# Optimization experiments

Measured on AMD Instinct MI355X. Metric: run time of the kernel, lower is better.

## Reference

```python
import jax, jax.numpy as jnp
import numpy as np

HEADS = 16
DIM_HEAD = 64


def rotate_half(t):
    x1, x2 = jnp.split(t, 2, axis=-1)
    return jnp.concatenate((-x2, x1), axis=-1)


def apply_rotary_pos_emb(t, freqs):
    # t: [b, h, n, l], freqs: [n, l]
    seq_len = t.shape[-2]
    freqs = freqs[-seq_len:, :]
    return t * jnp.cos(freqs) + rotate_half(t) * jnp.sin(freqs)


def setup_inputs() -> dict:
    key = jax.random.key(0)
    ks = jax.random.split(key, 6)
    b, n, dim, l = 2, 2048, 1024, 32
    x = jax.random.normal(ks[0], (b, n, dim), dtype=jnp.float32)
    rotary_pos_emb = jax.random.normal(ks[1], (n, l), dtype=jnp.float32)
    s = 0.02
    Wq = jax.random.normal(ks[2], (dim, dim), dtype=jnp.float32) * s
    Wk = jax.random.normal(ks[3], (dim, dim), dtype=jnp.float32) * s
    Wv = jax.random.normal(ks[4], (dim, dim), dtype=jnp.float32) * s
    Wout = jax.random.normal(ks[5], (dim, dim), dtype=jnp.float32) * s
    return {"x": x, "rotary_pos_emb": rotary_pos_emb, "Wq": Wq, "Wk": Wk, "Wv": Wv, "Wout": Wout}


def reference(x, rotary_pos_emb, Wq, Wk, Wv, Wout):
    b, n, _ = x.shape
    h, d = HEADS, DIM_HEAD
    scale = d ** -0.5

    def to_heads(t):
        return t.reshape(b, n, h, d).transpose(0, 2, 1, 3)  # b h n d

    q = to_heads(x @ Wq)
    k = to_heads(x @ Wk)
    v = to_heads(x @ Wv)

    # partial rotary on first l dims of q, k, v (module applies rope to v too)
    l = rotary_pos_emb.shape[-1]

    def rope(t):
        tl, tr = t[..., :l], t[..., l:]
        return jnp.concatenate((apply_rotary_pos_emb(tl, rotary_pos_emb), tr), axis=-1)

    q, k, v = rope(q), rope(k), rope(v)

    dots = jnp.einsum('bhid,bhjd->bhij', q, k) * scale  # [b, h, n, n]
    mask_value = jnp.finfo(dots.dtype).min
    causal = jnp.triu(jnp.ones((n, n), dtype=bool), k=1)  # i < j
    dots = jnp.where(causal[None, None, :, :], mask_value, dots)

    attn = jax.nn.softmax(dots, axis=-1)
    out = jnp.einsum('bhij,bhjd->bhid', attn, v)
    out = out.transpose(0, 2, 1, 3).reshape(b, n, h * d)  # b n (h d)
    return out @ Wout
```

## Files before the change

### kernel.cpp

```cpp
#include <hip/hip_runtime.h>
#include <hip/hip_bf16.h>
#include <stdint.h>

#define BATCH 2
#define SEQ 2048
#define NHEADS 16
#define DIM 1024
#define MTOT 4096
#define LOG2E 1.4426950408889634f
#define QSCALE (0.125f * LOG2E)
#define DEFER_THR 11.54f

typedef __attribute__((ext_vector_type(8))) short s16x8;
typedef __attribute__((ext_vector_type(4))) float f32x4;
typedef unsigned short u16;

__device__ __forceinline__ u16 f2b(float f) {
  union { float f; uint32_t u; } v; v.f = f;
  uint32_t r = v.u + 0x7FFFu + ((v.u >> 16) & 1u);
  return (u16)(r >> 16);
}
__device__ __forceinline__ u16 f2b_fast(float f) {
  union { float f; uint32_t u; } v; v.f = f;
  return (u16)((v.u + 0x8000u) >> 16);
}
__device__ __forceinline__ float b2f(u16 h) {
  union { uint32_t u; float f; } v; v.u = ((uint32_t)h) << 16;
  return v.f;
}

__device__ __forceinline__ void gload_lds16(void* lds, const void* g) {
  __builtin_amdgcn_global_load_lds(
      (const __attribute__((address_space(1))) unsigned int*)g,
      (__attribute__((address_space(3))) unsigned int*)lds, 16, 0, 0);
}

__global__ __launch_bounds__(256) void prep_kernel(
    const float* __restrict__ x, const float* __restrict__ Wq,
    const float* __restrict__ Wk, const float* __restrict__ Wv,
    const float* __restrict__ Wo, const float* __restrict__ rot,
    u16* __restrict__ xb, u16* __restrict__ WtAll, float2* __restrict__ cs) {
  __shared__ float tile[32][33];
  int bid = blockIdx.x, t = threadIdx.x;
  if (bid < 4096) {
    int i = (bid * 256 + t) * 4;
    float4 v = *(const float4*)(x + i);
    ushort4 o;
    o.x = f2b(v.x); o.y = f2b(v.y); o.z = f2b(v.z); o.w = f2b(v.w);
    *(ushort4*)(xb + i) = o;
  } else if (bid < 8192) {
    int bb = bid - 4096;
    int z = bb >> 10, xB = bb & 31, yB = (bb >> 5) & 31;
    const float* W = (z == 0) ? Wq : (z == 1) ? Wk : (z == 2) ? Wv : Wo;
    u16* Wt = WtAll + (size_t)z * DIM * DIM;
    int k0 = xB * 32, n0 = yB * 32;
    int tx = t & 31, ty = t >> 5;
#pragma unroll
    for (int i = 0; i < 4; i++) {
      int r = ty + i * 8;
      tile[r][tx] = W[(size_t)(k0 + r) * DIM + n0 + tx];
    }
    __syncthreads();
#pragma unroll
    for (int i = 0; i < 4; i++) {
      int r = ty + i * 8;
      Wt[(size_t)(n0 + r) * DIM + k0 + tx] = f2b(tile[tx][r]);
    }
  } else {
    int i = (bid - 8192) * 256 + t;
    float f = rot[i];
    float s, c;
    __sincosf(f, &s, &c);
    cs[i] = make_float2(c, s);
  }
}

template <int MODE>
__global__ __launch_bounds__(256) void gemm128(
    const u16* __restrict__ A, const u16* __restrict__ BtBase,
    void* __restrict__ Cbase, const float2* __restrict__ cs,
    u16* __restrict__ Qh, u16* __restrict__ Kh, u16* __restrict__ Vt) {
  __shared__ u16 Asm[2][128 * 32];
  __shared__ u16 Bsm[2][128 * 32];
  const u16* Bt = BtBase + (size_t)blockIdx.z * DIM * DIM;

  int t = threadIdx.x;
  int w = t >> 6, l = t & 63;
  int wr = w >> 1, wc = w & 1;
  int lr = l & 15, lg = l >> 4;
  int rowBase = blockIdx.x * 128;
  int colBase = blockIdx.y * 128;

  const char* Ab = (const char*)(A + (size_t)rowBase * DIM);
  const char* Bb = (const char*)(Bt + (size_t)colBase * DIM);

  f32x4 acc[4][4];
#pragma unroll
  for (int m = 0; m < 4; m++)
#pragma unroll
    for (int n = 0; n < 4; n++) acc[m][n] = (f32x4){0.f, 0.f, 0.f, 0.f};

  auto stage = [&](int buf, int kt) {
#pragma unroll
    for (int i = 0; i < 2; i++) {
      int ob = t * 16 + i * 4096;
      int row = ob >> 6, cb = ob & 63;
      int src = row * (DIM * 2) + kt * 64 + (cb ^ (((row >> 1) & 3) << 4));
      gload_lds16((char*)&Asm[buf][0] + ob, Ab + src);
      gload_lds16((char*)&Bsm[buf][0] + ob, Bb + src);
    }
  };

  stage(0, 0);
  for (int kt = 0; kt < DIM / 32; ++kt) {
    int cur = kt & 1;
    __syncthreads();
    if (kt + 1 < DIM / 32) stage(cur ^ 1, kt + 1);
    const char* ab = (const char*)&Asm[cur][0];
    const char* bb = (const char*)&Bsm[cur][0];
    s16x8 af[4], bf[4];
#pragma unroll
    for (int m = 0; m < 4; m++) {
      int R = wr * 64 + m * 16 + lr;
      af[m] = *(const s16x8*)(ab + R * 64 + ((lg * 16) ^ (((R >> 1) & 3) << 4)));
    }
#pragma unroll
    for (int n = 0; n < 4; n++) {
      int R = wc * 64 + n * 16 + lr;
      bf[n] = *(const s16x8*)(bb + R * 64 + ((lg * 16) ^ (((R >> 1) & 3) << 4)));
    }
    __builtin_amdgcn_s_setprio(1);
#pragma unroll
    for (int m = 0; m < 4; m++)
#pragma unroll
      for (int n = 0; n < 4; n++)
        acc[m][n] = __builtin_amdgcn_mfma_f32_16x16x32_bf16(af[m], bf[n], acc[m][n], 0, 0, 0);
    __builtin_amdgcn_s_setprio(0);
  }

  if constexpr (MODE == 1) {
    float* C = (float*)Cbase;
#pragma unroll
    for (int m = 0; m < 4; m++)
#pragma unroll
      for (int n = 0; n < 4; n++) {
        int row = rowBase + wr * 64 + m * 16 + lg * 4;
        int col = colBase + wc * 64 + n * 16 + lr;
#pragma unroll
        for (int r = 0; r < 4; r++)
          C[(size_t)(row + r) * DIM + col] = acc[m][n][r];
      }
  } else {
    int z = blockIdx.z;
    int h = (colBase + wc * 64) >> 6;
    if (z == 2) {
#pragma unroll
      for (int m = 0; m < 4; m++) {
#pragma unroll
        for (int r = 0; r < 4; r++) {
          int row = rowBase + wr * 64 + m * 16 + lg * 4 + r;
          int nrow = row & (SEQ - 1);
          int b2 = row >> 11;
          const float2* csr = cs + (size_t)nrow * 32;
          float a0 = acc[m][0][r], a1 = acc[m][1][r];
          float2 f0 = csr[lr];
          float2 f1 = csr[16 + lr];
          float o0 = a0 * f0.x - a1 * f0.y;
          float o1 = a1 * f1.x + a0 * f1.y;
          size_t vbase = ((size_t)(b2 * NHEADS + h) * 64) * SEQ + nrow;
          Vt[vbase + (size_t)lr * SEQ]        = f2b(o0);
          Vt[vbase + (size_t)(16 + lr) * SEQ] = f2b(o1);
          Vt[vbase + (size_t)(32 + lr) * SEQ] = f2b(acc[m][2][r]);
          Vt[vbase + (size_t)(48 + lr) * SEQ] = f2b(acc[m][3][r]);
        }
      }
    } else {
      u16* C = (z == 0) ? Qh : Kh;
      float sc = (z == 0) ? QSCALE : 1.0f;
#pragma unroll
      for (int m = 0; m < 4; m++) {
#pragma unroll
        for (int r = 0; r < 4; r++) {
          int row = rowBase + wr * 64 + m * 16 + lg * 4 + r;
          int nrow = row & (SEQ - 1);
          int b2 = row >> 11;
          const float2* csr = cs + (size_t)nrow * 32;
          float a0 = acc[m][0][r], a1 = acc[m][1][r];
          float2 f0 = csr[lr];
          float2 f1 = csr[16 + lr];
          float o0 = (a0 * f0.x - a1 * f0.y) * sc;
          float o1 = (a1 * f1.x + a0 * f1.y) * sc;
          size_t base = ((size_t)(b2 * NHEADS + h) * SEQ + nrow) * 64;
          C[base + lr]      = f2b(o0);
          C[base + 16 + lr] = f2b(o1);
          C[base + 32 + lr] = f2b(acc[m][2][r] * sc);
          C[base + 48 + lr] = f2b(acc[m][3][r] * sc);
        }
      }
    }
  }
}

__global__ __launch_bounds__(256) void attn_kernel(
    const u16* __restrict__ Qh, const u16* __restrict__ Kh,
    const u16* __restrict__ Vtg, u16* __restrict__ Ob) {
  int id = blockIdx.x;
  int xcd = id & 7, within = id >> 3;
  int bh = xcd * 4 + (within >> 4);
  int pi = within & 15;
  int b = bh >> 4, h = bh & 15;
  __shared__ u16 Ks[2][64 * 64];
  __shared__ u16 Vs[2][64 * 64];
  __shared__ u16 Ps[4][16 * 64];
  int t = threadIdx.x, w = t >> 6, l = t & 63;
  int lr = l & 15, lg = l >> 4;
  char* psb = (char*)&Ps[w][0];

  const char* Kbh = (const char*)(Kh + (size_t)bh * SEQ * 64);
  const char* Vbh = (const char*)Vtg + (size_t)bh * 64 * SEQ * 2;
  const u16* Qbh = Qh + (size_t)bh * SEQ * 64;

  auto stage = [&](int buf, int kt) {
    const char* kg = Kbh + (size_t)kt * 64 * 128;
    const char* vg = Vbh + kt * 128;
#pragma unroll
    for (int i = 0; i < 2; i++) {
      int ob = i * 4096 + t * 16;
      int row = ob >> 7, cb = ob & 127;
      int sw = cb ^ ((row & 7) << 4);
      gload_lds16((char*)&Ks[buf][0] + ob, kg + row * 128 + sw);
      gload_lds16((char*)&Vs[buf][0] + ob, vg + row * 4096 + sw);
    }
  };

#pragma unroll 1
  for (int ph = 0; ph < 2; ++ph) {
    int qt = ph ? (31 - pi) : pi;
    int nkt = qt + 1;
    int qrow0 = qt * 64 + w * 16;

    s16x8 qf[2];
#pragma unroll
    for (int kk = 0; kk < 2; kk++)
      qf[kk] = *(const s16x8*)(Qbh + (size_t)(qrow0 + lr) * 64 + kk * 32 + lg * 8);

    f32x4 o[4];
#pragma unroll
    for (int n = 0; n < 4; n++) o[n] = (f32x4){0.f, 0.f, 0.f, 0.f};
    float mrun[4], lsum[4];
#pragma unroll
    for (int r = 0; r < 4; r++) { mrun[r] = -3.0e38f; lsum[r] = 0.f; }

    __syncthreads();
    stage(0, 0);
    for (int kt = 0; kt < nkt; ++kt) {
      int cur = kt & 1;
      __syncthreads();
      if (kt + 1 < nkt) stage(cur ^ 1, kt + 1);
      const char* kb = (const char*)&Ks[cur][0];
      const char* vb = (const char*)&Vs[cur][0];

      f32x4 s[4];
#pragma unroll
      for (int n = 0; n < 4; n++) s[n] = (f32x4){0.f, 0.f, 0.f, 0.f};
      __builtin_amdgcn_s_setprio(1);
#pragma unroll
      for (int n = 0; n < 4; n++)
#pragma unroll
        for (int kk = 0; kk < 2; kk++) {
          int R = n * 16 + lr;
          s16x8 bk = *(const s16x8*)(kb + R * 128 + ((kk * 64 + lg * 16) ^ ((R & 7) << 4)));
          s[n] = __builtin_amdgcn_mfma_f32_16x16x32_bf16(qf[kk], bk, s[n], 0, 0, 0);
        }
      __builtin_amdgcn_s_setprio(0);

      if (kt == nkt - 1) {
#pragma unroll
        for (int n = 0; n < 4; n++) {
          int colg = kt * 64 + n * 16 + lr;
#pragma unroll
          for (int r = 0; r < 4; r++) {
            int rowg = qt * 64 + w * 16 + lg * 4 + r;
            if (colg > rowg) s[n][r] = -3.0e38f;
          }
        }
      }

      float tl[4];
#pragma unroll
      for (int r = 0; r < 4; r++)
        tl[r] = fmaxf(fmaxf(s[0][r], s[1][r]), fmaxf(s[2][r], s[3][r]));
      float need = fmaxf(fmaxf(tl[0] - mrun[0], tl[1] - mrun[1]),
                         fmaxf(tl[2] - mrun[2], tl[3] - mrun[3]));
      if (!__all(need <= DEFER_THR)) {
        float tm[4];
#pragma unroll
        for (int r = 0; r < 4; r++) tm[r] = tl[r];
#pragma unroll
        for (int off = 1; off < 16; off <<= 1)
#pragma unroll
          for (int r = 0; r < 4; r++) tm[r] = fmaxf(tm[r], __shfl_xor(tm[r], off, 64));
        float alpha[4];
#pragma unroll
        for (int r = 0; r < 4; r++) {
          float mn = fmaxf(mrun[r], tm[r]);
          alpha[r] = exp2f(mrun[r] - mn);
          mrun[r] = mn;
          lsum[r] *= alpha[r];
        }
#pragma unroll
        for (int n = 0; n < 4; n++)
#pragma unroll
          for (int r = 0; r < 4; r++) o[n][r] *= alpha[r];
      }
#pragma unroll
      for (int n = 0; n < 4; n++) {
#pragma unroll
        for (int r = 0; r < 4; r++) {
          float p = exp2f(s[n][r] - mrun[r]);
          lsum[r] += p;
          int prow = lg * 4 + r;
          *(u16*)(psb + prow * 128 + (((n * 16 + lr) * 2) ^ ((prow & 7) << 4))) = f2b_fast(p);
        }
      }

      s16x8 pa[2];
#pragma unroll
      for (int kk = 0; kk < 2; kk++)
        pa[kk] = *(const s16x8*)(psb + lr * 128 + ((kk * 64 + lg * 16) ^ ((lr & 7) << 4)));
      __builtin_amdgcn_s_setprio(1);
#pragma unroll
      for (int n = 0; n < 4; n++)
#pragma unroll
        for (int kk = 0; kk < 2; kk++) {
          int R = n * 16 + lr;
          s16x8 vv = *(const s16x8*)(vb + R * 128 + ((kk * 64 + lg * 16) ^ ((R & 7) << 4)));
          o[n] = __builtin_amdgcn_mfma_f32_16x16x32_bf16(pa[kk], vv, o[n], 0, 0, 0);
        }
      __builtin_amdgcn_s_setprio(0);
    }

#pragma unroll
    for (int off = 1; off < 16; off <<= 1)
#pragma unroll
      for (int r = 0; r < 4; r++) lsum[r] += __shfl_xor(lsum[r], off, 64);
    float inv[4];
#pragma unroll
    for (int r = 0; r < 4; r++) inv[r] = 1.0f / lsum[r];
#pragma unroll
    for (int n = 0; n < 4; n++)
#pragma unroll
      for (int r = 0; r < 4; r++) {
        int rowg = qt * 64 + w * 16 + lg * 4 + r;
        int col = h * 64 + n * 16 + lr;
        Ob[((size_t)b * SEQ + rowg) * DIM + col] = f2b(o[n][r] * inv[r]);
      }
  }
}

extern "C" void kernel_launch(void* const* d_in, const int* in_sizes, int n_in,
                              void* d_out, int out_size, void* d_ws, size_t ws_size,
                              hipStream_t stream) {
  (void)in_sizes; (void)n_in; (void)out_size; (void)ws_size;
  const float* x = (const float*)d_in[0];
  const float* rot = (const float*)d_in[1];
  const float* Wq = (const float*)d_in[2];
  const float* Wk = (const float*)d_in[3];
  const float* Wv = (const float*)d_in[4];
  const float* Wo = (const float*)d_in[5];

  char* ws = (char*)d_ws;
  u16* xb    = (u16*)(ws);
  u16* WtAll = (u16*)(ws + (8ll << 20));
  u16* Qh    = (u16*)(ws + (16ll << 20));
  u16* Kh    = (u16*)(ws + (24ll << 20));
  u16* Vt    = (u16*)(ws + (32ll << 20));
  u16* Ob    = (u16*)(ws + (40ll << 20));
  float2* cs = (float2*)(ws + (48ll << 20));

  prep_kernel<<<8448, 256, 0, stream>>>(x, Wq, Wk, Wv, Wo, rot, xb, WtAll, cs);
  gemm128<0><<<dim3(32, 8, 3), 256, 0, stream>>>(xb, WtAll, nullptr, cs, Qh, Kh, Vt);
  attn_kernel<<<512, 256, 0, stream>>>(Qh, Kh, Vt, Ob);
  gemm128<1><<<dim3(32, 8, 1), 256, 0, stream>>>(Ob, WtAll + 3ll * DIM * DIM, d_out,
                                                 nullptr, nullptr, nullptr, nullptr);
}
```

Measured before the change: 212.5 us.

## Replace QKV GEMM with 256x256-tile 8-wave pipelined kernel

The fused QKV projection now uses a dedicated kernel with 256x256 output tiles, 512 threads and a K-step of 64. Each K-step is split into half-tile stages that are issued interleaved with the MFMA phases under explicit barriers and vmcnt waits. The grid shrinks from 768 to 192 blocks, and each block treats the three weight matrices as one 3072-wide B operand. This is meant to raise data reuse per LDS load and overlap global loads with compute. The cost is fewer blocks than the 256 CUs on the device, so the single wave of work may leave CUs idle, along with higher register and LDS pressure.

After: 199.5 us. -6.1%, faster.

```diff
diff --git a/kernel.cpp b/kernel.cpp
--- a/kernel.cpp
+++ b/kernel.cpp
@@ -75,22 +75,181 @@
   }
 }
 
-template <int MODE>
-__global__ __launch_bounds__(256) void gemm128(
-    const u16* __restrict__ A, const u16* __restrict__ BtBase,
-    void* __restrict__ Cbase, const float2* __restrict__ cs,
-    u16* __restrict__ Qh, u16* __restrict__ Kh, u16* __restrict__ Vt) {
+#define NKT 16
+__global__ __launch_bounds__(512, 2) void qkv8_kernel(
+    const u16* __restrict__ A, const u16* __restrict__ Bt,
+    const float2* __restrict__ cs, u16* __restrict__ Qh,
+    u16* __restrict__ Kh, u16* __restrict__ Vt) {
+  __shared__ u16 lds[2][4][8192];
+  const int t = threadIdx.x;
+  const int w = t >> 6, l = t & 63;
+  const int wr = w >> 2, wc = w & 3;
+  const int lr = l & 15, lg = l >> 4;
+  const int rowBase = blockIdx.x * 256;
+  const int colBase = blockIdx.y * 256;
+  const char* Ab = (const char*)(A + (size_t)rowBase * DIM);
+  const char* Bb = (const char*)(Bt + (size_t)colBase * DIM);
+  const int t16 = t * 16;
+  const int swz = ((lr >> 1) & 3) << 4;
+
+  f32x4 acc[8][4];
+#pragma unroll
+  for (int m = 0; m < 8; m++)
+#pragma unroll
+    for (int n = 0; n < 4; n++) acc[m][n] = (f32x4){0.f, 0.f, 0.f, 0.f};
+
+  auto stageH = [&](int buf, int kind, int kt) {
+    const char* gb = (kind >= 2) ? Bb : Ab;
+    int khalf = kind & 1;
+    char* ldst = (char*)&lds[buf][kind][0];
+#pragma unroll
+    for (int i = 0; i < 2; i++) {
+      int ob = t16 + i * 8192;
+      int row = ob >> 6, cb = ob & 63;
+      gload_lds16(ldst + ob,
+                  gb + (size_t)row * (DIM * 2) + kt * 128 + khalf * 64 +
+                      (cb ^ (((row >> 1) & 3) << 4)));
+    }
+  };
+  auto rdA = [&](int cur, int m, int kk) -> s16x8 {
+    int R = wr * 128 + m * 16 + lr;
+    return *(const s16x8*)((const char*)&lds[cur][kk][0] + R * 64 + ((lg * 16) ^ swz));
+  };
+  auto rdB = [&](int cur, int n, int kk) -> s16x8 {
+    int R = wc * 64 + n * 16 + lr;
+    return *(const s16x8*)((const char*)&lds[cur][2 + kk][0] + R * 64 + ((lg * 16) ^ swz));
+  };
+
+  stageH(0, 0, 0); stageH(0, 2, 0); stageH(0, 1, 0); stageH(0, 3, 0);
+  stageH(1, 2, 1); stageH(1, 0, 1); stageH(1, 3, 1);
+
+  for (int kt = 0; kt < NKT; ++kt) {
+    const int cur = kt & 1, nxt = cur ^ 1;
+    if (kt >= NKT - 2) { asm volatile("s_waitcnt vmcnt(0)" ::: "memory"); }
+    else               { asm volatile("s_waitcnt vmcnt(6)" ::: "memory"); }
+    __builtin_amdgcn_s_barrier();
+    __builtin_amdgcn_sched_barrier(0);
+
+    s16x8 af[4], bf[4];
+#pragma unroll
+    for (int i = 0; i < 4; i++) { af[i] = rdA(cur, i, 0); bf[i] = rdB(cur, i, 0); }
+    if (kt + 1 < NKT) stageH(nxt, 1, kt + 1);
+    __builtin_amdgcn_s_barrier();
+    __builtin_amdgcn_sched_barrier(0);
+    __builtin_amdgcn_s_setprio(1);
+#pragma unroll
+    for (int m = 0; m < 4; m++)
+#pragma unroll
+      for (int n = 0; n < 4; n++)
+        acc[m][n] = __builtin_amdgcn_mfma_f32_16x16x32_bf16(af[m], bf[n], acc[m][n], 0, 0, 0);
+    __builtin_amdgcn_s_setprio(0);
+    __builtin_amdgcn_s_barrier();
+    __builtin_amdgcn_sched_barrier(0);
+#pragma unroll
+    for (int i = 0; i < 4; i++) af[i] = rdA(cur, 4 + i, 0);
+    if (kt + 2 < NKT) stageH(cur, 2, kt + 2);
+    __builtin_amdgcn_s_barrier();
+    __builtin_amdgcn_sched_barrier(0);
+    __builtin_amdgcn_s_setprio(1);
+#pragma unroll
+    for (int m = 0; m < 4; m++)
+#pragma unroll
+      for (int n = 0; n < 4; n++)
+        acc[4 + m][n] = __builtin_amdgcn_mfma_f32_16x16x32_bf16(af[m], bf[n], acc[4 + m][n], 0, 0, 0);
+    __builtin_amdgcn_s_setprio(0);
+    __builtin_amdgcn_s_barrier();
+    __builtin_amdgcn_sched_barrier(0);
+#pragma unroll
+    for (int i = 0; i < 4; i++) { af[i] = rdA(cur, i, 1); bf[i] = rdB(cur, i, 1); }
+    if (kt + 2 < NKT) stageH(cur, 0, kt + 2);
+    __builtin_amdgcn_s_barrier();
+    __builtin_amdgcn_sched_barrier(0);
+    __builtin_amdgcn_s_setprio(1);
+#pragma unroll
+    for (int m = 0; m < 4; m++)
+#pragma unroll
+      for (int n = 0; n < 4; n++)
+        acc[m][n] = __builtin_amdgcn_mfma_f32_16x16x32_bf16(af[m], bf[n], acc[m][n], 0, 0, 0);
+    __builtin_amdgcn_s_setprio(0);
+    __builtin_amdgcn_s_barrier();
+    __builtin_amdgcn_sched_barrier(0);
+#pragma unroll
+    for (int i = 0; i < 4; i++) af[i] = rdA(cur, 4 + i, 1);
+    if (kt + 2 < NKT) stageH(cur, 3, kt + 2);
+    __builtin_amdgcn_s_barrier();
+    __builtin_amdgcn_sched_barrier(0);
+    __builtin_amdgcn_s_setprio(1);
+#pragma unroll
+    for (int m = 0; m < 4; m++)
+#pragma unroll
+      for (int n = 0; n < 4; n++)
+        acc[4 + m][n] = __builtin_amdgcn_mfma_f32_16x16x32_bf16(af[m], bf[n], acc[4 + m][n], 0, 0, 0);
+    __builtin_amdgcn_s_setprio(0);
+    __builtin_amdgcn_s_barrier();
+    __builtin_amdgcn_sched_barrier(0);
+  }
+
+  int cg = colBase + wc * 64;
+  int z = cg >> 10;
+  int h = (cg >> 6) & (NHEADS - 1);
+  if (z == 2) {
+#pragma unroll
+    for (int m = 0; m < 8; m++) {
+#pragma unroll
+      for (int r = 0; r < 4; r++) {
+        int row = rowBase + wr * 128 + m * 16 + lg * 4 + r;
+        int nrow = row & (SEQ - 1);
+        int b2 = row >> 11;
+        const float2* csr = cs + (size_t)nrow * 32;
+        float a0 = acc[m][0][r], a1 = acc[m][1][r];
+        float2 f0 = csr[lr];
+        float2 f1 = csr[16 + lr];
+        float o0 = a0 * f0.x - a1 * f0.y;
+        float o1 = a1 * f1.x + a0 * f1.y;
+        size_t vbase = ((size_t)(b2 * NHEADS + h) * 64) * SEQ + nrow;
+        Vt[vbase + (size_t)lr * SEQ]        = f2b(o0);
+        Vt[vbase + (size_t)(16 + lr) * SEQ] = f2b(o1);
+        Vt[vbase + (size_t)(32 + lr) * SEQ] = f2b(acc[m][2][r]);
+        Vt[vbase + (size_t)(48 + lr) * SEQ] = f2b(acc[m][3][r]);
+      }
+    }
+  } else {
+    u16* C = (z == 0) ? Qh : Kh;
+    float sc = (z == 0) ? QSCALE : 1.0f;
+#pragma unroll
+    for (int m = 0; m < 8; m++) {
+#pragma unroll
+      for (int r = 0; r < 4; r++) {
+        int row = rowBase + wr * 128 + m * 16 + lg * 4 + r;
+        int nrow = row & (SEQ - 1);
+        int b2 = row >> 11;
+        const float2* csr = cs + (size_t)nrow * 32;
+        float a0 = acc[m][0][r], a1 = acc[m][1][r];
+        float2 f0 = csr[lr];
+        float2 f1 = csr[16 + lr];
+        float o0 = (a0 * f0.x - a1 * f0.y) * sc;
+        float o1 = (a1 * f1.x + a0 * f1.y) * sc;
+        size_t base = ((size_t)(b2 * NHEADS + h) * SEQ + nrow) * 64;
+        C[base + lr]      = f2b(o0);
+        C[base + 16 + lr] = f2b(o1);
+        C[base + 32 + lr] = f2b(acc[m][2][r] * sc);
+        C[base + 48 + lr] = f2b(acc[m][3][r] * sc);
+      }
+    }
+  }
+}
+
+__global__ __launch_bounds__(256) void gemm_out(
+    const u16* __restrict__ A, const u16* __restrict__ Bt,
+    float* __restrict__ C) {
   __shared__ u16 Asm[2][128 * 32];
   __shared__ u16 Bsm[2][128 * 32];
-  const u16* Bt = BtBase + (size_t)blockIdx.z * DIM * DIM;
-
   int t = threadIdx.x;
   int w = t >> 6, l = t & 63;
   int wr = w >> 1, wc = w & 1;
   int lr = l & 15, lg = l >> 4;
   int rowBase = blockIdx.x * 128;
   int colBase = blockIdx.y * 128;
-
   const char* Ab = (const char*)(A + (size_t)rowBase * DIM);
   const char* Bb = (const char*)(Bt + (size_t)colBase * DIM);
 
@@ -138,67 +297,16 @@
     __builtin_amdgcn_s_setprio(0);
   }
 
-  if constexpr (MODE == 1) {
-    float* C = (float*)Cbase;
-#pragma unroll
-    for (int m = 0; m < 4; m++)
-#pragma unroll
-      for (int n = 0; n < 4; n++) {
-        int row = rowBase + wr * 64 + m * 16 + lg * 4;
-        int col = colBase + wc * 64 + n * 16 + lr;
-#pragma unroll
-        for (int r = 0; r < 4; r++)
-          C[(size_t)(row + r) * DIM + col] = acc[m][n][r];
-      }
-  } else {
-    int z = blockIdx.z;
-    int h = (colBase + wc * 64) >> 6;
-    if (z == 2) {
-#pragma unroll
-      for (int m = 0; m < 4; m++) {
-#pragma unroll
-        for (int r = 0; r < 4; r++) {
-          int row = rowBase + wr * 64 + m * 16 + lg * 4 + r;
-          int nrow = row & (SEQ - 1);
-          int b2 = row >> 11;
-          const float2* csr = cs + (size_t)nrow * 32;
-          float a0 = acc[m][0][r], a1 = acc[m][1][r];
-          float2 f0 = csr[lr];
-          float2 f1 = csr[16 + lr];
-          float o0 = a0 * f0.x - a1 * f0.y;
-          float o1 = a1 * f1.x + a0 * f1.y;
-          size_t vbase = ((size_t)(b2 * NHEADS + h) * 64) * SEQ + nrow;
-          Vt[vbase + (size_t)lr * SEQ]        = f2b(o0);
-          Vt[vbase + (size_t)(16 + lr) * SEQ] = f2b(o1);
-          Vt[vbase + (size_t)(32 + lr) * SEQ] = f2b(acc[m][2][r]);
-          Vt[vbase + (size_t)(48 + lr) * SEQ] = f2b(acc[m][3][r]);
-        }
-      }
-    } else {
-      u16* C = (z == 0) ? Qh : Kh;
-      float sc = (z == 0) ? QSCALE : 1.0f;
-#pragma unroll
-      for (int m = 0; m < 4; m++) {
-#pragma unroll
-        for (int r = 0; r < 4; r++) {
-          int row = rowBase + wr * 64 + m * 16 + lg * 4 + r;
-          int nrow = row & (SEQ - 1);
-          int b2 = row >> 11;
-          const float2* csr = cs + (size_t)nrow * 32;
-          float a0 = acc[m][0][r], a1 = acc[m][1][r];
-          float2 f0 = csr[lr];
-          float2 f1 = csr[16 + lr];
-          float o0 = (a0 * f0.x - a1 * f0.y) * sc;
-          float o1 = (a1 * f1.x + a0 * f1.y) * sc;
-          size_t base = ((size_t)(b2 * NHEADS + h) * SEQ + nrow) * 64;
-          C[base + lr]      = f2b(o0);
-          C[base + 16 + lr] = f2b(o1);
-          C[base + 32 + lr] = f2b(acc[m][2][r] * sc);
-          C[base + 48 + lr] = f2b(acc[m][3][r] * sc);
-        }
-      }
-    }
-  }
+#pragma unroll
+  for (int m = 0; m < 4; m++)
+#pragma unroll
+    for (int n = 0; n < 4; n++) {
+      int row = rowBase + wr * 64 + m * 16 + lg * 4;
+      int col = colBase + wc * 64 + n * 16 + lr;
+#pragma unroll
+      for (int r = 0; r < 4; r++)
+        C[(size_t)(row + r) * DIM + col] = acc[m][n][r];
+    }
 }
 
 __global__ __launch_bounds__(256) void attn_kernel(
@@ -379,8 +487,7 @@
   float2* cs = (float2*)(ws + (48ll << 20));
 
   prep_kernel<<<8448, 256, 0, stream>>>(x, Wq, Wk, Wv, Wo, rot, xb, WtAll, cs);
-  gemm128<0><<<dim3(32, 8, 3), 256, 0, stream>>>(xb, WtAll, nullptr, cs, Qh, Kh, Vt);
+  qkv8_kernel<<<dim3(16, 12), 512, 0, stream>>>(xb, WtAll, cs, Qh, Kh, Vt);
   attn_kernel<<<512, 256, 0, stream>>>(Qh, Kh, Vt, Ob);
-  gemm128<1><<<dim3(32, 8, 1), 256, 0, stream>>>(Ob, WtAll + 3ll * DIM * DIM, d_out,
-                                                 nullptr, nullptr, nullptr, nullptr);
-}
+  gemm_out<<<dim3(32, 8), 256, 0, stream>>>(Ob, WtAll + 3ll * DIM * DIM, (float*)d_out);
+}
```
